# Optimization experiments

Measured on AMD Instinct MI355X. Metric: run time of the kernel, lower is better.

Reference implementation:

```python
import jax, jax.numpy as jnp
import numpy as np

N = 50000   # nodes
E = 800000  # edges (avg degree 16)
D = 128     # in_channels == num_hidden_channels


def setup_inputs() -> dict:
    key = jax.random.key(0)
    ks = jax.random.split(key, 8)
    embs = jax.random.normal(ks[0], (N, D), dtype=jnp.float32)
    edge_index0 = jax.random.randint(ks[1], (2, E), 0, N)
    edge_index1 = jax.random.randint(ks[2], (2, E), 0, N)
    s = 1.0 / np.sqrt(D)  # torch Linear default init bound
    Wl0 = jax.random.uniform(ks[3], (D, D), jnp.float32, -s, s)
    Wr0 = jax.random.uniform(ks[4], (D, D), jnp.float32, -s, s)
    bl0 = jax.random.uniform(ks[5], (D,), jnp.float32, -s, s)
    Wl1 = jax.random.uniform(ks[6], (D, D), jnp.float32, -s, s)
    Wr1 = jax.random.uniform(ks[7], (D, D), jnp.float32, -s, s)
    bl1 = jnp.zeros((D,), jnp.float32)
    return {"embs": embs, "edge_index0": edge_index0, "edge_index1": edge_index1,
            "Wl0": Wl0, "bl0": bl0, "Wr0": Wr0, "Wl1": Wl1, "bl1": bl1, "Wr1": Wr1}


def sage_conv(x, edge_index, Wl, bl, Wr):
    # PyG SAGEConv, aggr='mean': out = lin_l(mean_{j->i} x_j) + lin_r(x_i)
    src, dst = edge_index[0], edge_index[1]
    msg = x[src]  # [E, D] gather of source-node features
    agg = jax.ops.segment_sum(msg, dst, num_segments=x.shape[0])            # [N, D]
    cnt = jax.ops.segment_sum(jnp.ones((src.shape[0],), x.dtype), dst,
                              num_segments=x.shape[0])                      # [N]
    mean = agg / jnp.maximum(cnt, 1.0)[:, None]  # isolated nodes -> 0 (scatter_mean)
    return mean @ Wl + bl + x @ Wr


def reference(embs, edge_index0, edge_index1, Wl0, bl0, Wr0, Wl1, bl1, Wr1):
    # outer layer 0 (not last) -> conv, dropout (eval: identity), exact GELU
    x = sage_conv(embs, edge_index0, Wl0, bl0, Wr0)
    x = jax.nn.gelu(x, approximate=False)
    # outer layer 1 (last) -> conv only
    x = sage_conv(x, edge_index1, Wl1, bl1, Wr1)
    return x
```

## Files before the change

### kernel.cpp

```cpp
#include <hip/hip_runtime.h>
#include <math.h>

#define D 128
#define BKT_SHIFT 8
#define CHUNK 4096
#define CAP 5120

typedef __attribute__((ext_vector_type(8))) short bf8;
typedef __attribute__((ext_vector_type(4))) float f4;

__device__ __forceinline__ float b2f(ushort u) {
    union { uint i; float f; } x; x.i = ((uint)u) << 16; return x.f;
}
__device__ __forceinline__ ushort f2b(float f) {
    union { float f; uint i; } x; x.f = f;
    uint i = x.i;
    i += 0x7fffu + ((i >> 16) & 1u);
    return (ushort)(i >> 16);
}

__global__ __launch_bounds__(256)
void prep_fused(const float* __restrict__ embs, ushort* __restrict__ xb, long n4,
                const float* __restrict__ W0, const float* __restrict__ W1,
                const float* __restrict__ W2, const float* __restrict__ W3,
                ushort* __restrict__ WT, int* __restrict__ gbc) {
    const int t = threadIdx.x;
    if (blockIdx.x < 4) {
        __shared__ ushort s[128][132];
        const float* W = blockIdx.x == 0 ? W0 : blockIdx.x == 1 ? W1 : blockIdx.x == 2 ? W2 : W3;
        ushort* o = WT + (long)blockIdx.x * D * D;
        if (blockIdx.x == 0) { gbc[t] = 0; gbc[256 + t] = 0; }
        for (int i = t; i < D * D; i += 256) { int k = i >> 7, c = i & 127; s[k][c] = f2b(W[i]); }
        __syncthreads();
        for (int i = t; i < D * D; i += 256) { int c = i >> 7, k = i & 127; o[i] = s[k][c]; }
        return;
    }
    long i = (long)(blockIdx.x - 4) * blockDim.x + t;
    long stride = (long)(gridDim.x - 4) * blockDim.x;
    for (; i < n4; i += stride) {
        float4 v = ((const float4*)embs)[i];
        ushort4 o = { f2b(v.x), f2b(v.y), f2b(v.z), f2b(v.w) };
        ((ushort4*)xb)[i] = o;
    }
}

__global__ __launch_bounds__(256)
void bucket_scatter(const int* __restrict__ ei0, const int* __restrict__ ei1, int E,
                    int* __restrict__ gbc, uint* __restrict__ tmpf) {
    const int* ei = blockIdx.y ? ei1 : ei0;
    int* cnts = gbc + blockIdx.y * 256;
    uint* tp = tmpf + (size_t)blockIdx.y * 256 * CAP;
    __shared__ int lhist[256], lstart[256], lcur[256], gbase[256];
    __shared__ int ws[4];
    __shared__ uint sw[CHUNK];
    const int t = threadIdx.x;
    const int e0 = blockIdx.x * CHUNK;
    const int cnt = min(CHUNK, E - e0);
    lhist[t] = 0;
    __syncthreads();
    for (int i = t; i < cnt; i += 256)
        atomicAdd(&lhist[ei[E + e0 + i] >> BKT_SHIFT], 1);
    __syncthreads();
    {
        int lane = t & 63, wid = t >> 6;
        int v = lhist[t];
        int incl = v;
        #pragma unroll
        for (int o = 1; o < 64; o <<= 1) { int u = __shfl_up(incl, o); if (lane >= o) incl += u; }
        if (lane == 63) ws[wid] = incl;
        __syncthreads();
        int wb = 0;
        #pragma unroll
        for (int w = 0; w < 3; ++w) if (w < wid) wb += ws[w];
        int excl = incl - v + wb;
        lstart[t] = excl;
        lcur[t] = excl;
    }
    __syncthreads();
    for (int i = t; i < cnt; i += 256) {
        int s = ei[e0 + i];
        int d = ei[E + e0 + i];
        int r = atomicAdd(&lcur[d >> BKT_SHIFT], 1);
        sw[r] = ((uint)d << 16) | (uint)s;
    }
    __syncthreads();
    gbase[t] = lhist[t] > 0 ? atomicAdd(&cnts[t], lhist[t]) : 0;
    __syncthreads();
    for (int i = t; i < cnt; i += 256) {
        uint w = sw[i];
        int b = w >> 24;
        tp[(size_t)b * CAP + gbase[b] + (i - lstart[b])] = w;
    }
}

__global__ __launch_bounds__(256)
void exact_place(const uint* __restrict__ tmpf, const int* __restrict__ gbc,
                 int* __restrict__ o0, int* __restrict__ o1,
                 int* __restrict__ d0, int* __restrict__ d1,
                 ushort* __restrict__ s0, ushort* __restrict__ s1, int N) {
    const int layer = blockIdx.y;
    const uint* tp = tmpf + ((size_t)layer * 256 + blockIdx.x) * CAP;
    int* offs = layer ? o1 : o0;
    int* deg  = layer ? d1 : d0;
    ushort* srcs = layer ? s1 : s0;
    __shared__ int lh[256], lc[256], sbase[256];
    __shared__ int ws[4];
    const int t = threadIdx.x;
    const int lane = t & 63, wid = t >> 6;
    const int node0 = blockIdx.x << BKT_SHIFT;

    {
        int v = gbc[layer * 256 + t];
        int incl = v;
        #pragma unroll
        for (int o = 1; o < 64; o <<= 1) { int u = __shfl_up(incl, o); if (lane >= o) incl += u; }
        if (lane == 63) ws[wid] = incl;
        __syncthreads();
        int wb = 0;
        #pragma unroll
        for (int w = 0; w < 3; ++w) if (w < wid) wb += ws[w];
        sbase[t] = incl - v + wb;
        lh[t] = 0;
    }
    __syncthreads();
    const int bstart = sbase[blockIdx.x];
    const int cnt = gbc[layer * 256 + blockIdx.x];

    for (int i = t; i < cnt; i += 256)
        atomicAdd(&lh[(tp[i] >> 16) & 255], 1);
    __syncthreads();
    {
        int v = lh[t];
        int incl = v;
        #pragma unroll
        for (int o = 1; o < 64; o <<= 1) { int u = __shfl_up(incl, o); if (lane >= o) incl += u; }
        if (lane == 63) ws[wid] = incl;
        __syncthreads();
        int wb = 0;
        #pragma unroll
        for (int w = 0; w < 3; ++w) if (w < wid) wb += ws[w];
        int excl = incl - v + wb;
        int node = node0 + t;
        if (node < N) { offs[node] = bstart + excl; deg[node] = v; }
        lc[t] = bstart + excl;
    }
    __syncthreads();
    for (int i = t; i < cnt; i += 256) {
        uint w = tp[i];
        int p = atomicAdd(&lc[(w >> 16) & 255], 1);
        srcs[p] = (ushort)(w & 0xffff);
    }
}

__global__ void gather_mean_b(const ushort* __restrict__ xb, const ushort* __restrict__ srcs,
                              const int* __restrict__ offs, const int* __restrict__ deg,
                              ushort* __restrict__ meanb, int N) {
    int node = blockIdx.x * (blockDim.x >> 6) + (threadIdx.x >> 6);
    if (node >= N) return;
    int lane = threadIdx.x & 63;
    int g = lane >> 4;
    int c = (lane & 15) * 8;
    int beg = offs[node], dc = deg[node];
    int end = beg + dc;
    float a[8] = {0.f, 0.f, 0.f, 0.f, 0.f, 0.f, 0.f, 0.f};
    int e = beg + g;
    for (; e + 12 < end; e += 16) {
        int s0 = srcs[e];
        int s1 = srcs[e + 4];
        int s2 = srcs[e + 8];
        int s3 = srcs[e + 12];
        bf8 v0 = *(const bf8*)(xb + (long)s0 * D + c);
        bf8 v1 = *(const bf8*)(xb + (long)s1 * D + c);
        bf8 v2 = *(const bf8*)(xb + (long)s2 * D + c);
        bf8 v3 = *(const bf8*)(xb + (long)s3 * D + c);
        #pragma unroll
        for (int q = 0; q < 8; ++q)
            a[q] += (b2f((ushort)v0[q]) + b2f((ushort)v1[q]))
                  + (b2f((ushort)v2[q]) + b2f((ushort)v3[q]));
    }
    for (; e + 4 < end; e += 8) {
        int s0 = srcs[e];
        int s1 = srcs[e + 4];
        bf8 v0 = *(const bf8*)(xb + (long)s0 * D + c);
        bf8 v1 = *(const bf8*)(xb + (long)s1 * D + c);
        #pragma unroll
        for (int q = 0; q < 8; ++q) a[q] += b2f((ushort)v0[q]) + b2f((ushort)v1[q]);
    }
    if (e < end) {
        int s0 = srcs[e];
        bf8 v0 = *(const bf8*)(xb + (long)s0 * D + c);
        #pragma unroll
        for (int q = 0; q < 8; ++q) a[q] += b2f((ushort)v0[q]);
    }
    #pragma unroll
    for (int q = 0; q < 8; ++q) {
        a[q] += __shfl_xor(a[q], 16);
        a[q] += __shfl_xor(a[q], 32);
    }
    if (g == 0) {
        float inv = dc > 0 ? 1.0f / (float)dc : 0.0f;
        bf8 o;
        #pragma unroll
        for (int q = 0; q < 8; ++q) o[q] = (short)f2b(a[q] * inv);
        *(bf8*)(meanb + (long)node * D + c) = o;
    }
}

template <int ACT>
__global__ __launch_bounds__(512)
void gemm_mfma(const ushort* __restrict__ meanb, const ushort* __restrict__ xb,
               const ushort* __restrict__ WTl, const ushort* __restrict__ WTr,
               const float* __restrict__ bias, float* __restrict__ outf,
               ushort* __restrict__ outb, int N) {
    __shared__ ushort sW[2 * D * D];
    const int t = threadIdx.x;
    const int lane = t & 63;
    const int wid  = t >> 6;

    #pragma unroll
    for (int i = 0; i < 8; ++i) {
        const ushort* Wsrc = (i < 4) ? WTl : WTr;
        int off = (t << 4) + (i & 3) * 8192;
        int row = off >> 8;
        int dst = ((i < 4) ? 0 : 32768) + (off ^ ((row & 7) << 4));
        *(bf8*)((char*)sW + dst) = *(const bf8*)((const char*)Wsrc + off);
    }

    const int r0   = blockIdx.x * 256 + wid * 32;
    const int arow = r0 + (lane & 15);
    const int kg   = lane >> 4;
    bf8 z = {};
    bf8 am[8], ax[8];
    #pragma unroll
    for (int m = 0; m < 4; ++m) {
        const long a0 = (long)arow * D + kg * 8 + m * 32;
        if (arow < N)      { am[m]   = *(const bf8*)(meanb + a0);
                             ax[m]   = *(const bf8*)(xb + a0); }
        else               { am[m]   = z; ax[m]   = z; }
        if (arow + 16 < N) { am[m+4] = *(const bf8*)(meanb + a0 + 16 * D);
                             ax[m+4] = *(const bf8*)(xb + a0 + 16 * D); }
        else               { am[m+4] = z; ax[m+4] = z; }
    }

    const int sxor = (lane & 7) << 4;
    int p[4];
    #pragma unroll
    for (int m = 0; m < 4; ++m)
        p[m] = (lane & 15) * 256 + ((kg * 16 + m * 64) ^ sxor);

    __syncthreads();

    f4 acc0[8], acc1[8];
    #pragma unroll
    for (int n = 0; n < 8; ++n) { acc0[n] = (f4){0.f,0.f,0.f,0.f}; acc1[n] = (f4){0.f,0.f,0.f,0.f}; }

    #pragma unroll
    for (int m = 0; m < 4; ++m) {
        #pragma unroll
        for (int n = 0; n < 8; ++n) {
            bf8 bl = *(const bf8*)((const char*)sW + n * 4096 + p[m]);
            acc0[n] = __builtin_amdgcn_mfma_f32_16x16x32_bf16(am[m],     bl, acc0[n], 0, 0, 0);
            acc1[n] = __builtin_amdgcn_mfma_f32_16x16x32_bf16(am[m + 4], bl, acc1[n], 0, 0, 0);
        }
    }
    #pragma unroll
    for (int m = 0; m < 4; ++m) {
        #pragma unroll
        for (int n = 0; n < 8; ++n) {
            bf8 br = *(const bf8*)((const char*)sW + 32768 + n * 4096 + p[m]);
            acc0[n] = __builtin_amdgcn_mfma_f32_16x16x32_bf16(ax[m],     br, acc0[n], 0, 0, 0);
            acc1[n] = __builtin_amdgcn_mfma_f32_16x16x32_bf16(ax[m + 4], br, acc1[n], 0, 0, 0);
        }
    }

    const int col0  = lane & 15;
    const int orow0 = r0 + kg * 4;
    #pragma unroll
    for (int n = 0; n < 8; ++n) {
        const int col = n * 16 + col0;
        const float b = bias[col];
        #pragma unroll
        for (int r = 0; r < 4; ++r) {
            #pragma unroll
            for (int h = 0; h < 2; ++h) {
                const int row = orow0 + r + h * 16;
                if (row >= N) continue;
                float v = (h ? acc1[n][r] : acc0[n][r]) + b;
                if (ACT) {
                    v = 0.5f * v * (1.0f + erff(v * 0.70710678118654752f));
                    outb[(long)row * D + col] = f2b(v);
                } else {
                    outf[(long)row * D + col] = v;
                }
            }
        }
    }
}

extern "C" void kernel_launch(void* const* d_in, const int* in_sizes, int n_in,
                              void* d_out, int out_size, void* d_ws, size_t ws_size,
                              hipStream_t stream) {
    const float* embs = (const float*)d_in[0];
    const int*   ei0  = (const int*)d_in[1];
    const int*   ei1  = (const int*)d_in[2];
    const float* Wl0  = (const float*)d_in[3];
    const float* bl0  = (const float*)d_in[4];
    const float* Wr0  = (const float*)d_in[5];
    const float* Wl1  = (const float*)d_in[6];
    const float* bl1  = (const float*)d_in[7];
    const float* Wr1  = (const float*)d_in[8];

    const int N = in_sizes[0] / D;
    const int E = in_sizes[1] / 2;
    float* out = (float*)d_out;

    char* w = (char*)d_ws;
    ushort* xb    = (ushort*)w;  w += (size_t)N * D * 2;
    ushort* meanb = (ushort*)w;  w += (size_t)N * D * 2;
    ushort* WT    = (ushort*)w;  w += (size_t)4 * D * D * 2;
    int* gbc      = (int*)w;     w += 512 * 4;
    int* offs0    = (int*)w;     w += (size_t)N * 4;
    int* offs1    = (int*)w;     w += (size_t)N * 4;
    int* deg0     = (int*)w;     w += (size_t)N * 4;
    int* deg1     = (int*)w;     w += (size_t)N * 4;
    uint* tmpf    = (uint*)w;    w += (size_t)2 * 256 * CAP * 4;
    ushort* srcs0 = (ushort*)w;  w += (size_t)E * 2;
    ushort* srcs1 = (ushort*)w;

    ushort* WTl0 = WT;
    ushort* WTr0 = WT + D * D;
    ushort* WTl1 = WT + 2 * D * D;
    ushort* WTr1 = WT + 3 * D * D;

    const int nbkt = (N + 255) >> BKT_SHIFT;
    const int ncnk = (E + CHUNK - 1) / CHUNK;
    const int ab   = (N + 3) / 4;
    const int gb   = (N + 255) / 256;

    prep_fused<<<2052, 256, 0, stream>>>(embs, xb, (long)N * D / 4,
                                         Wl0, Wr0, Wl1, Wr1, WT, gbc);

    bucket_scatter<<<dim3(ncnk, 2), 256, 0, stream>>>(ei0, ei1, E, gbc, tmpf);
    exact_place<<<dim3(nbkt, 2), 256, 0, stream>>>(tmpf, gbc, offs0, offs1,
                                                   deg0, deg1, srcs0, srcs1, N);

    gather_mean_b<<<ab, 256, 0, stream>>>(xb, srcs0, offs0, deg0, meanb, N);
    gemm_mfma<1><<<gb, 512, 0, stream>>>(meanb, xb, WTl0, WTr0, bl0, nullptr, xb, N);

    gather_mean_b<<<ab, 256, 0, stream>>>(xb, srcs1, offs1, deg1, meanb, N);
    gemm_mfma<0><<<gb, 512, 0, stream>>>(meanb, xb, WTl1, WTr1, bl1, out, nullptr, N);
}
```

Baseline: 141.3 us.

## Fuse prep into bucket scatter, pre-swizzle weights, use direct LDS loads in GEMM

```diff
diff --git a/kernel.cpp b/kernel.cpp
--- a/kernel.cpp
+++ b/kernel.cpp
@@ -19,41 +19,63 @@
     return (ushort)(i >> 16);
 }
 
+__global__ void zero_gbc(int* __restrict__ gbc) { gbc[threadIdx.x] = 0; }
+
 __global__ __launch_bounds__(256)
-void prep_fused(const float* __restrict__ embs, ushort* __restrict__ xb, long n4,
-                const float* __restrict__ W0, const float* __restrict__ W1,
-                const float* __restrict__ W2, const float* __restrict__ W3,
-                ushort* __restrict__ WT, int* __restrict__ gbc) {
+void prep_scatter(const int* __restrict__ ei0, const int* __restrict__ ei1, int E,
+                  int* __restrict__ gbc, uint* __restrict__ tmpf,
+                  const float* __restrict__ embs, ushort* __restrict__ xb, long n4,
+                  const float* __restrict__ Wl0, const float* __restrict__ Wr0,
+                  const float* __restrict__ Wl1, const float* __restrict__ Wr1,
+                  ushort* __restrict__ WTsw) {
+    __shared__ char smem[4112 + CHUNK * 4];
     const int t = threadIdx.x;
-    if (blockIdx.x < 4) {
-        __shared__ ushort s[128][132];
-        const float* W = blockIdx.x == 0 ? W0 : blockIdx.x == 1 ? W1 : blockIdx.x == 2 ? W2 : W3;
-        ushort* o = WT + (long)blockIdx.x * D * D;
-        if (blockIdx.x == 0) { gbc[t] = 0; gbc[256 + t] = 0; }
-        for (int i = t; i < D * D; i += 256) { int k = i >> 7, c = i & 127; s[k][c] = f2b(W[i]); }
-        __syncthreads();
-        for (int i = t; i < D * D; i += 256) { int c = i >> 7, k = i & 127; o[i] = s[k][c]; }
+
+    if (blockIdx.y == 2) {
+        if (blockIdx.x < 4) {
+            const float* Wsrc = blockIdx.x == 0 ? Wl0 : blockIdx.x == 1 ? Wr0
+                               : blockIdx.x == 2 ? Wl1 : Wr1;
+            ushort* dstm = WTsw + (size_t)blockIdx.x * D * D;
+            ushort (*tile)[33] = (ushort(*)[33])smem;
+            const int r  = t >> 3;
+            const int c0 = (t & 7) * 4;
+            for (int tt = 0; tt < 16; ++tt) {
+                int ti = tt >> 2, tj = tt & 3;
+                float4 v = *(const float4*)(Wsrc + (ti * 32 + r) * D + tj * 32 + c0);
+                tile[r][c0 + 0] = f2b(v.x);
+                tile[r][c0 + 1] = f2b(v.y);
+                tile[r][c0 + 2] = f2b(v.z);
+                tile[r][c0 + 3] = f2b(v.w);
+                __syncthreads();
+                int row = tj * 32 + r;
+                int off = row * 256 + (ti * 32 + c0) * 2;
+                int doff = off ^ ((row & 7) << 4);
+                ushort4 o = { tile[c0 + 0][r], tile[c0 + 1][r],
+                              tile[c0 + 2][r], tile[c0 + 3][r] };
+                *(ushort4*)((char*)dstm + doff) = o;
+                __syncthreads();
+            }
+            return;
+        }
+        long i = (long)(blockIdx.x - 4) * 256 + t;
+        long stride = (long)(gridDim.x - 4) * 256;
+        for (; i < n4; i += stride) {
+            float4 v = ((const float4*)embs)[i];
+            ushort4 o = { f2b(v.x), f2b(v.y), f2b(v.z), f2b(v.w) };
+            ((ushort4*)xb)[i] = o;
+        }
         return;
     }
-    long i = (long)(blockIdx.x - 4) * blockDim.x + t;
-    long stride = (long)(gridDim.x - 4) * blockDim.x;
-    for (; i < n4; i += stride) {
-        float4 v = ((const float4*)embs)[i];
-        ushort4 o = { f2b(v.x), f2b(v.y), f2b(v.z), f2b(v.w) };
-        ((ushort4*)xb)[i] = o;
-    }
-}
-
-__global__ __launch_bounds__(256)
-void bucket_scatter(const int* __restrict__ ei0, const int* __restrict__ ei1, int E,
-                    int* __restrict__ gbc, uint* __restrict__ tmpf) {
+
+    int* lhist  = (int*)smem;
+    int* lstart = (int*)(smem + 1024);
+    int* lcur   = (int*)(smem + 2048);
+    int* gbase  = (int*)(smem + 3072);
+    int* ws     = (int*)(smem + 4096);
+    uint* sw    = (uint*)(smem + 4112);
     const int* ei = blockIdx.y ? ei1 : ei0;
     int* cnts = gbc + blockIdx.y * 256;
     uint* tp = tmpf + (size_t)blockIdx.y * 256 * CAP;
-    __shared__ int lhist[256], lstart[256], lcur[256], gbase[256];
-    __shared__ int ws[4];
-    __shared__ uint sw[CHUNK];
-    const int t = threadIdx.x;
     const int e0 = blockIdx.x * CHUNK;
     const int cnt = min(CHUNK, E - e0);
     lhist[t] = 0;
@@ -207,9 +229,9 @@
 }
 
 template <int ACT>
-__global__ __launch_bounds__(512)
+__global__ __launch_bounds__(256, 2)
 void gemm_mfma(const ushort* __restrict__ meanb, const ushort* __restrict__ xb,
-               const ushort* __restrict__ WTl, const ushort* __restrict__ WTr,
+               const ushort* __restrict__ WTsw,
                const float* __restrict__ bias, float* __restrict__ outf,
                ushort* __restrict__ outb, int N) {
     __shared__ ushort sW[2 * D * D];
@@ -217,16 +239,20 @@
     const int lane = t & 63;
     const int wid  = t >> 6;
 
-    #pragma unroll
-    for (int i = 0; i < 8; ++i) {
-        const ushort* Wsrc = (i < 4) ? WTl : WTr;
-        int off = (t << 4) + (i & 3) * 8192;
-        int row = off >> 8;
-        int dst = ((i < 4) ? 0 : 32768) + (off ^ ((row & 7) << 4));
-        *(bf8*)((char*)sW + dst) = *(const bf8*)((const char*)Wsrc + off);
-    }
-
-    const int r0   = blockIdx.x * 256 + wid * 32;
+    {
+        const char* src = (const char*)WTsw;
+        char* dst = (char*)sW;
+        #pragma unroll
+        for (int i = 0; i < 16; ++i) {
+            int off = i * 4096 + t * 16;
+            __builtin_amdgcn_global_load_lds(
+                (const __attribute__((address_space(1))) unsigned int*)(src + off),
+                (__attribute__((address_space(3))) unsigned int*)(dst + off),
+                16, 0, 0);
+        }
+    }
+
+    const int r0   = blockIdx.x * 128 + wid * 32;
     const int arow = r0 + (lane & 15);
     const int kg   = lane >> 4;
     bf8 z = {};
@@ -327,26 +353,21 @@
     ushort* srcs0 = (ushort*)w;  w += (size_t)E * 2;
     ushort* srcs1 = (ushort*)w;
 
-    ushort* WTl0 = WT;
-    ushort* WTr0 = WT + D * D;
-    ushort* WTl1 = WT + 2 * D * D;
-    ushort* WTr1 = WT + 3 * D * D;
-
     const int nbkt = (N + 255) >> BKT_SHIFT;
     const int ncnk = (E + CHUNK - 1) / CHUNK;
     const int ab   = (N + 3) / 4;
-    const int gb   = (N + 255) / 256;
-
-    prep_fused<<<2052, 256, 0, stream>>>(embs, xb, (long)N * D / 4,
-                                         Wl0, Wr0, Wl1, Wr1, WT, gbc);
-
-    bucket_scatter<<<dim3(ncnk, 2), 256, 0, stream>>>(ei0, ei1, E, gbc, tmpf);
+    const int gb   = (N + 127) / 128;
+
+    zero_gbc<<<1, 512, 0, stream>>>(gbc);
+    prep_scatter<<<dim3(ncnk, 3), 256, 0, stream>>>(ei0, ei1, E, gbc, tmpf,
+                                                    embs, xb, (long)N * D / 4,
+                                                    Wl0, Wr0, Wl1, Wr1, WT);
     exact_place<<<dim3(nbkt, 2), 256, 0, stream>>>(tmpf, gbc, offs0, offs1,
                                                    deg0, deg1, srcs0, srcs1, N);
 
     gather_mean_b<<<ab, 256, 0, stream>>>(xb, srcs0, offs0, deg0, meanb, N);
-    gemm_mfma<1><<<gb, 512, 0, stream>>>(meanb, xb, WTl0, WTr0, bl0, nullptr, xb, N);
+    gemm_mfma<1><<<gb, 256, 0, stream>>>(meanb, xb, WT, bl0, nullptr, xb, N);
 
     gather_mean_b<<<ab, 256, 0, stream>>>(xb, srcs1, offs1, deg1, meanb, N);
-    gemm_mfma<0><<<gb, 512, 0, stream>>>(meanb, xb, WTl1, WTr1, bl1, out, nullptr, N);
-}
+    gemm_mfma<0><<<gb, 256, 0, stream>>>(meanb, xb, WT + 2 * D * D, bl1, out, nullptr, N);
+}
```

Result: no change. 141.3 us (-0.0%).
